# Optimization experiments

Measured on AMD Instinct MI355X. Metric: run time of the kernel, lower is better.

The kernel has to match this reference:

```python
import jax, jax.numpy as jnp
import numpy as np
from jax.ops import segment_sum

N_NODES = 100000
N_EDGES = 3200000
IN_DIM = 128
HID = 128
INT_DIM = 512
OUT_DIM = 3


def gcn_conv(x, W, b, src, dst, n):
    # PyG GCNConv (eval): add self-loops, symmetric normalization, aggregate, bias.
    loop = jnp.arange(n, dtype=src.dtype)
    s = jnp.concatenate([src, loop])
    d = jnp.concatenate([dst, loop])
    deg = segment_sum(jnp.ones_like(d, dtype=x.dtype), d, num_segments=n)  # [N]
    dinv = jnp.where(deg > 0, jax.lax.rsqrt(jnp.maximum(deg, 1e-12)), 0.0)
    norm = dinv[s] * dinv[d]                      # [E+N]
    h = x @ W                                      # [N, F_out]
    msg = h[s] * norm[:, None]                    # gather + scale
    return segment_sum(msg, d, num_segments=n) + b


def setup_inputs() -> dict:
    key = jax.random.key(0)
    ks = jax.random.split(key, 12)
    def lin(kw, kb, fi, fo):
        lim = 1.0 / np.sqrt(fi)
        W = jax.random.uniform(kw, (fi, fo), jnp.float32, -lim, lim)
        b = jax.random.uniform(kb, (fo,), jnp.float32, -lim, lim)
        return W, b
    x = jax.random.normal(ks[0], (N_NODES, IN_DIM), jnp.float32)
    edge_index = jax.random.randint(ks[1], (2, N_EDGES), 0, N_NODES, dtype=jnp.int64)
    W1, b1 = lin(ks[2], ks[3], IN_DIM, HID)
    W2, b2 = lin(ks[4], ks[5], HID, HID)
    W3, b3 = lin(ks[6], ks[7], HID, INT_DIM)
    Wi, bi = lin(ks[8], ks[9], INT_DIM, INT_DIM)
    Wc, bc = lin(ks[10], ks[11], INT_DIM, OUT_DIM)
    return {"x": x, "edge_index": edge_index, "W1": W1, "b1": b1, "W2": W2,
            "b2": b2, "W3": W3, "b3": b3, "Wi": Wi, "bi": bi, "Wc": Wc, "bc": bc}


def reference(x, edge_index, W1, b1, W2, b2, W3, b3, Wi, bi, Wc, bc):
    src, dst = edge_index[0], edge_index[1]
    n = x.shape[0]
    h = jax.nn.relu(gcn_conv(x, W1, b1, src, dst, n))
    h = jax.nn.relu(gcn_conv(h, W2, b2, src, dst, n))
    h = jax.nn.relu(gcn_conv(h, W3, b3, src, dst, n))
    h = jax.nn.relu(h @ Wi + bi)
    return h @ Wc + bc
```

## Files before the change

### kernel.cpp

```cpp
#include <hip/hip_runtime.h>
#include <hip/hip_fp16.h>

#define NN 100000
#define NE 3200000
#define NB 391
#define NBLK 512
#define EPB 6250

typedef unsigned int uint32;
typedef unsigned short u16;
typedef long long ll64;
typedef __attribute__((ext_vector_type(8))) _Float16 half8;
typedef __attribute__((ext_vector_type(4))) float f32x4;

__device__ inline float2 h2f2(uint32 u) {
  __half2 h = *reinterpret_cast<__half2*>(&u);
  return __half22float2(h);
}
__device__ inline uint32 f2h2(float x, float y) {
  return (uint32)__half_as_ushort(__float2half(x)) |
         ((uint32)__half_as_ushort(__float2half(y)) << 16);
}
__device__ inline int edge_at(const void* ei, int is64, ll64 idx) {
  return is64 ? (int)((const ll64*)ei)[idx] : ((const int*)ei)[idx];
}
__device__ inline int detect64(const int* ei32) {
  int acc = 0;
#pragma unroll
  for (int k = 1; k < 32; k += 2) acc |= ei32[k];
  return (acc == 0) ? 1 : 0;
}

__global__ __launch_bounds__(256) void k_binB(const void* __restrict__ ei,
                                              int* __restrict__ tbl) {
  __shared__ int h[NB];
  __shared__ int sIs64;
  int k = blockIdx.x, tid = threadIdx.x;
  for (int i = tid; i < NB; i += 256) h[i] = 0;
  if (tid == 0) sIs64 = detect64((const int*)ei);
  __syncthreads();
  int is64 = sIs64;
  ll64 beg = (ll64)k * EPB, end = beg + EPB;
  for (ll64 i = beg + tid; i < end; i += 256)
    atomicAdd(&h[edge_at(ei, is64, (ll64)NE + i) >> 8], 1);
  __syncthreads();
  for (int i = tid; i < NB; i += 256) tbl[k * NB + i] = h[i];
}
__global__ __launch_bounds__(512) void k_binC1(int* __restrict__ tbl,
                                               int* __restrict__ total) {
  __shared__ int sd[NBLK];
  int b = blockIdx.x, tid = threadIdx.x;
  int v = tbl[tid * NB + b];
  sd[tid] = v;
  __syncthreads();
  for (int off = 1; off < NBLK; off <<= 1) {
    int t = (tid >= off) ? sd[tid - off] : 0;
    __syncthreads();
    sd[tid] += t;
    __syncthreads();
  }
  tbl[tid * NB + b] = sd[tid] - v;
  if (tid == NBLK - 1) total[b] = sd[NBLK - 1];
}
__global__ __launch_bounds__(512) void k_binC2(const int* __restrict__ total,
                                               int* __restrict__ bbase,
                                               int* __restrict__ offs) {
  __shared__ int sd[512];
  int tid = threadIdx.x;
  int v = (tid < NB) ? total[tid] : 0;
  sd[tid] = v;
  __syncthreads();
  for (int off = 1; off < 512; off <<= 1) {
    int t = (tid >= off) ? sd[tid - off] : 0;
    __syncthreads();
    sd[tid] += t;
    __syncthreads();
  }
  if (tid < NB) bbase[tid] = sd[tid] - v;
  if (tid == 0) offs[NN] = NE;
}
__global__ __launch_bounds__(256) void k_binD(const void* __restrict__ ei,
                                              const int* __restrict__ tbl,
                                              const int* __restrict__ bbase,
                                              uint32* __restrict__ binned) {
  __shared__ int lb[NB];
  __shared__ int lc[NB];
  __shared__ int sIs64;
  int k = blockIdx.x, tid = threadIdx.x;
  for (int i = tid; i < NB; i += 256) {
    lb[i] = tbl[k * NB + i] + bbase[i];
    lc[i] = 0;
  }
  if (tid == 0) sIs64 = detect64((const int*)ei);
  __syncthreads();
  int is64 = sIs64;
  ll64 beg = (ll64)k * EPB, end = beg + EPB;
  for (ll64 i = beg + tid; i < end; i += 256) {
    int s = edge_at(ei, is64, i);
    int d = edge_at(ei, is64, (ll64)NE + i);
    int b = d >> 8;
    int r = atomicAdd(&lc[b], 1);
    binned[lb[b] + r] = (uint32)s | ((uint32)(d & 255) << 24);
  }
}
__global__ __launch_bounds__(256) void k_binE(const uint32* __restrict__ binned,
                                              const int* __restrict__ bbase,
                                              const int* __restrict__ total,
                                              int* __restrict__ offs,
                                              float* __restrict__ dinv,
                                              int* __restrict__ csr) {
  __shared__ int cnt[256], pref[256], fil[256];
  int b = blockIdx.x, tid = threadIdx.x;
  cnt[tid] = 0;
  fil[tid] = 0;
  __syncthreads();
  int base = bbase[b], tot = total[b];
  for (int i = tid; i < tot; i += 256) atomicAdd(&cnt[binned[base + i] >> 24], 1);
  __syncthreads();
  int v = cnt[tid];
  pref[tid] = v;
  __syncthreads();
  for (int off = 1; off < 256; off <<= 1) {
    int t = (tid >= off) ? pref[tid - off] : 0;
    __syncthreads();
    pref[tid] += t;
    __syncthreads();
  }
  int myoff = pref[tid] - v;
  pref[tid] = myoff;
  int node = b * 256 + tid;
  if (node < NN) {
    offs[node] = base + myoff;
    dinv[node] = rsqrtf((float)(v + 1));
  }
  __syncthreads();
  for (int i = tid; i < tot; i += 256) {
    uint32 w = binned[base + i];
    int dl = w >> 24;
    int r = atomicAdd(&fil[dl], 1);
    csr[base + pref[dl] + r] = (int)(w & 0xFFFFFFu);
  }
}

__device__ inline void packOne(const float* __restrict__ W, u16* __restrict__ ph,
                               int K, int N, int t) {
  int j = t & 7, lane = (t >> 3) & 63, tl = t >> 9;
  int kbn = K >> 5;
  int kb = tl % kbn, ntile = tl / kbn;
  int k = kb * 32 + (lane >> 4) * 8 + j;
  int n2 = ntile * 16 + (lane & 15);
  ph[t] = __half_as_ushort(__float2half(W[k * N + n2]));
}
__global__ void k_packhalf(const float* W1, const float* W2, const float* W3,
                           const float* Wi, u16* p1, u16* p2, u16* p3, u16* pi,
                           const float4* __restrict__ x, ushort4* __restrict__ xh,
                           const float* __restrict__ dinv) {
  int t = blockIdx.x * blockDim.x + threadIdx.x;
  if (t < 16384) packOne(W1, p1, 128, 128, t);
  else if (t < 32768) packOne(W2, p2, 128, 128, t - 16384);
  else if (t < 98304) packOne(W3, p3, 128, 512, t - 32768);
  else if (t < 360448) packOne(Wi, pi, 512, 512, t - 98304);
  else {
    int i = t - 360448;
    if (i < NN * 32) {
      float4 v = x[i];
      float sc = dinv[i >> 5];
      ushort4 o;
      o.x = __half_as_ushort(__float2half(v.x * sc));
      o.y = __half_as_ushort(__float2half(v.y * sc));
      o.z = __half_as_ushort(__float2half(v.z * sc));
      o.w = __half_as_ushort(__float2half(v.w * sc));
      xh[i] = o;
    }
  }
}

__device__ inline void agg32_phase0(const u16* __restrict__ xin,
                                    const int* __restrict__ csr,
                                    const int* __restrict__ offs,
                                    const float* __restrict__ dinv,
                                    int row0, int tid, u16* __restrict__ tile) {
  int lane = tid & 63, wave = tid >> 6;
  int sub = lane >> 4, fl = lane & 15;
  const uint4* xv = (const uint4*)xin;
#pragma unroll
  for (int rnd = 0; rnd < 2; rnd++) {
    int nloc = rnd * 16 + wave * 4 + sub;
    int node = row0 + nloc;
    int beg = offs[node], end = offs[node + 1];
    float acc[8] = {};
    int j = beg;
    for (; j + 7 < end; j += 8) {
      int s[8];
      uint4 r[8];
#pragma unroll
      for (int q = 0; q < 8; q++) s[q] = csr[j + q];
#pragma unroll
      for (int q = 0; q < 8; q++) r[q] = xv[(ll64)s[q] * 16 + fl];
#pragma unroll
      for (int q = 0; q < 8; q++) {
        float2 p0 = h2f2(r[q].x), p1 = h2f2(r[q].y);
        float2 p2 = h2f2(r[q].z), p3 = h2f2(r[q].w);
        acc[0] += p0.x; acc[1] += p0.y; acc[2] += p1.x; acc[3] += p1.y;
        acc[4] += p2.x; acc[5] += p2.y; acc[6] += p3.x; acc[7] += p3.y;
      }
    }
    for (; j + 3 < end; j += 4) {
      int s[4];
      uint4 r[4];
#pragma unroll
      for (int q = 0; q < 4; q++) s[q] = csr[j + q];
#pragma unroll
      for (int q = 0; q < 4; q++) r[q] = xv[(ll64)s[q] * 16 + fl];
#pragma unroll
      for (int q = 0; q < 4; q++) {
        float2 p0 = h2f2(r[q].x), p1 = h2f2(r[q].y);
        float2 p2 = h2f2(r[q].z), p3 = h2f2(r[q].w);
        acc[0] += p0.x; acc[1] += p0.y; acc[2] += p1.x; acc[3] += p1.y;
        acc[4] += p2.x; acc[5] += p2.y; acc[6] += p3.x; acc[7] += p3.y;
      }
    }
    for (; j < end; j++) {
      uint4 r = xv[(ll64)csr[j] * 16 + fl];
      float2 p0 = h2f2(r.x), p1 = h2f2(r.y), p2 = h2f2(r.z), p3 = h2f2(r.w);
      acc[0] += p0.x; acc[1] += p0.y; acc[2] += p1.x; acc[3] += p1.y;
      acc[4] += p2.x; acc[5] += p2.y; acc[6] += p3.x; acc[7] += p3.y;
    }
    float di = dinv[node];
    uint4 sf = xv[(ll64)node * 16 + fl];
    float2 q0 = h2f2(sf.x), q1 = h2f2(sf.y), q2 = h2f2(sf.z), q3 = h2f2(sf.w);
    uint4 ov;
    ov.x = f2h2(di * (acc[0] + q0.x), di * (acc[1] + q0.y));
    ov.y = f2h2(di * (acc[2] + q1.x), di * (acc[3] + q1.y));
    ov.z = f2h2(di * (acc[4] + q2.x), di * (acc[5] + q2.y));
    ov.w = f2h2(di * (acc[6] + q3.x), di * (acc[7] + q3.y));
    *(uint4*)&tile[nloc * 128 + ((fl ^ (nloc & 7)) << 3)] = ov;
  }
}

__device__ inline void load_af(const u16* __restrict__ tile, int lane,
                               half8 af[2][4]) {
  int quad = (lane >> 4), l16 = lane & 15;
#pragma unroll
  for (int rt = 0; rt < 2; rt++) {
    int row = rt * 16 + l16;
#pragma unroll
    for (int kb = 0; kb < 4; kb++)
      af[rt][kb] = *(const half8*)&tile[row * 128 + (((kb * 4 + quad) ^ (row & 7)) << 3)];
  }
}

__global__ __launch_bounds__(256, 4) void k_fusedL(
    const u16* __restrict__ xin, const int* __restrict__ csr,
    const int* __restrict__ offs, const float* __restrict__ dinv,
    const u16* __restrict__ Wp, const float* __restrict__ bias,
    u16* __restrict__ Co) {
  __shared__ u16 tile[32 * 128];
  int tid = threadIdx.x;
  int wave = tid >> 6, lane = tid & 63, quad = lane >> 4, l16 = lane & 15;
  int row0 = blockIdx.x * 32;
  agg32_phase0(xin, csr, offs, dinv, row0, tid, tile);
  __syncthreads();
  half8 af[2][4];
  load_af(tile, lane, af);
#pragma unroll
  for (int p = 0; p < 2; p++) {
    int nt = wave * 2 + p;
    half8 bv[4];
#pragma unroll
    for (int kb = 0; kb < 4; kb++)
      bv[kb] = *(const half8*)&Wp[((ll64)(nt * 4 + kb) * 64 + lane) * 8];
    f32x4 acc0 = {0, 0, 0, 0}, acc1 = {0, 0, 0, 0};
#pragma unroll
    for (int kb = 0; kb < 4; kb++) {
      acc0 = __builtin_amdgcn_mfma_f32_16x16x32_f16(af[0][kb], bv[kb], acc0, 0, 0, 0);
      acc1 = __builtin_amdgcn_mfma_f32_16x16x32_f16(af[1][kb], bv[kb], acc1, 0, 0, 0);
    }
    int col = nt * 16 + l16;
    float bvv = bias[col];
#pragma unroll
    for (int r = 0; r < 4; r++) {
      int r0 = quad * 4 + r, r1 = r0 + 16;
      Co[(ll64)(row0 + r0) * 128 + col] =
          __half_as_ushort(__float2half(fmaxf(acc0[r] + bvv, 0.0f) * dinv[row0 + r0]));
      Co[(ll64)(row0 + r1) * 128 + col] =
          __half_as_ushort(__float2half(fmaxf(acc1[r] + bvv, 0.0f) * dinv[row0 + r1]));
    }
  }
}

__global__ __launch_bounds__(256, 4) void k_tail32f(
    const u16* __restrict__ xin, const int* __restrict__ csr,
    const int* __restrict__ offs, const float* __restrict__ dinv,
    const u16* __restrict__ W3p, const float* __restrict__ b3,
    const u16* __restrict__ Wip, const float* __restrict__ bi,
    const float* __restrict__ Wc, const float* __restrict__ bc,
    float* __restrict__ out, int M) {
  __shared__ u16 h3s[32 * 512];
  __shared__ float sRed[4][32][3];
  int tid = threadIdx.x;
  int wave = tid >> 6, lane = tid & 63, quad = lane >> 4, l16 = lane & 15;
  int row0 = blockIdx.x * 32;

  agg32_phase0(xin, csr, offs, dinv, row0, tid, h3s);
  __syncthreads();
  half8 af[2][4];
  load_af(h3s, lane, af);
  __syncthreads();

  {
    f32x4 acc0 = {0, 0, 0, 0}, acc1 = {0, 0, 0, 0};
    half8 bq[4];
#pragma unroll
    for (int p = 0; p < 3; p++)
      bq[p] = *(const half8*)&W3p[((ll64)(wave * 32 + p) * 64 + lane) * 8];
#pragma unroll 4
    for (int t = 0; t < 32; t++) {
      if (t + 3 < 32)
        bq[(t + 3) & 3] = *(const half8*)&W3p[((ll64)(wave * 32 + t + 3) * 64 + lane) * 8];
      half8 bcur = bq[t & 3];
      int kb = t & 3;
      acc0 = __builtin_amdgcn_mfma_f32_16x16x32_f16(af[0][kb], bcur, acc0, 0, 0, 0);
      acc1 = __builtin_amdgcn_mfma_f32_16x16x32_f16(af[1][kb], bcur, acc1, 0, 0, 0);
      if (kb == 3) {
        int nt = wave * 8 + (t >> 2);
        int col = nt * 16 + l16;
        float bv = b3[col];
#pragma unroll
        for (int r = 0; r < 4; r++) {
          int row0l = quad * 4 + r;
          float v0 = fmaxf(acc0[r] + bv, 0.0f);
          float v1 = fmaxf(acc1[r] + bv, 0.0f);
          int oct0 = (col >> 3) ^ (row0l & 7);
          h3s[row0l * 512 + oct0 * 8 + (col & 7)] = __half_as_ushort(__float2half(v0));
          int row1l = 16 + row0l;
          int oct1 = (col >> 3) ^ (row1l & 7);
          h3s[row1l * 512 + oct1 * 8 + (col & 7)] = __half_as_ushort(__float2half(v1));
        }
        acc0 = (f32x4){0, 0, 0, 0};
        acc1 = (f32x4){0, 0, 0, 0};
      }
    }
  }
  __syncthreads();

  float acc3[2][4][3] = {};
  {
    f32x4 acc0 = {0, 0, 0, 0}, acc1 = {0, 0, 0, 0};
    half8 bq[4];
#pragma unroll
    for (int p = 0; p < 3; p++)
      bq[p] = *(const half8*)&Wip[((ll64)(wave * 128 + p) * 64 + lane) * 8];
    int r0l = l16, r1l = 16 + l16;
    int sw0 = r0l & 7;
#pragma unroll 4
    for (int t = 0; t < 128; t++) {
      if (t + 3 < 128)
        bq[(t + 3) & 3] = *(const half8*)&Wip[((ll64)(wave * 128 + t + 3) * 64 + lane) * 8];
      half8 bcur = bq[t & 3];
      int kb = t & 15;
      int oct = ((kb * 4 + quad) ^ sw0);
      half8 a0 = *(const half8*)&h3s[r0l * 512 + oct * 8];
      half8 a1 = *(const half8*)&h3s[r1l * 512 + oct * 8];
      acc0 = __builtin_amdgcn_mfma_f32_16x16x32_f16(a0, bcur, acc0, 0, 0, 0);
      acc1 = __builtin_amdgcn_mfma_f32_16x16x32_f16(a1, bcur, acc1, 0, 0, 0);
      if (kb == 15) {
        int nt = wave * 8 + (t >> 4);
        int col = nt * 16 + l16;
        float bv = bi[col];
        float w0 = Wc[col * 3 + 0], w1 = Wc[col * 3 + 1], w2 = Wc[col * 3 + 2];
#pragma unroll
        for (int r = 0; r < 4; r++) {
          float v0 = fmaxf(acc0[r] + bv, 0.0f);
          float v1 = fmaxf(acc1[r] + bv, 0.0f);
          acc3[0][r][0] += v0 * w0; acc3[0][r][1] += v0 * w1; acc3[0][r][2] += v0 * w2;
          acc3[1][r][0] += v1 * w0; acc3[1][r][1] += v1 * w1; acc3[1][r][2] += v1 * w2;
        }
        acc0 = (f32x4){0, 0, 0, 0};
        acc1 = (f32x4){0, 0, 0, 0};
      }
    }
  }
#pragma unroll
  for (int rt = 0; rt < 2; rt++)
#pragma unroll
    for (int r = 0; r < 4; r++)
#pragma unroll
      for (int c = 0; c < 3; c++) {
        float v = acc3[rt][r][c];
        v += __shfl_xor(v, 1);
        v += __shfl_xor(v, 2);
        v += __shfl_xor(v, 4);
        v += __shfl_xor(v, 8);
        acc3[rt][r][c] = v;
      }
  if (l16 == 0) {
#pragma unroll
    for (int rt = 0; rt < 2; rt++)
#pragma unroll
      for (int r = 0; r < 4; r++)
#pragma unroll
        for (int c = 0; c < 3; c++)
          sRed[wave][rt * 16 + quad * 4 + r][c] = acc3[rt][r][c];
  }
  __syncthreads();
  if (tid < 96) {
    int row = tid / 3, c = tid % 3;
    out[(ll64)(row0 + row) * 3 + c] = sRed[0][row][c] + sRed[1][row][c] +
                                      sRed[2][row][c] + sRed[3][row][c] + bc[c];
  }
}

extern "C" void kernel_launch(void* const* d_in, const int* in_sizes, int n_in,
                              void* d_out, int out_size, void* d_ws, size_t ws_size,
                              hipStream_t stream) {
  const float* x  = (const float*)d_in[0];
  const void*  ei = d_in[1];
  const float* W1 = (const float*)d_in[2];
  const float* b1 = (const float*)d_in[3];
  const float* W2 = (const float*)d_in[4];
  const float* b2 = (const float*)d_in[5];
  const float* W3 = (const float*)d_in[6];
  const float* b3 = (const float*)d_in[7];
  const float* Wi = (const float*)d_in[8];
  const float* bi = (const float*)d_in[9];
  const float* Wc = (const float*)d_in[10];
  const float* bc = (const float*)d_in[11];
  float* out = (float*)d_out;

  char* ws = (char*)d_ws;
  const ll64 KB = 1ll << 10, MB = 1ll << 20;
  float* dinv  = (float*)(ws + 0);
  int*   offs  = (int*)(ws + 512 * KB);
  int*   total = (int*)(ws + 1 * MB + 64 * KB);
  int*   bbase = (int*)(ws + 1 * MB + 128 * KB);
  int*   tbl   = (int*)(ws + 1 * MB + 192 * KB);
  uint32* binned = (uint32*)(ws + 2 * MB);
  int*   csr   = (int*)(ws + 15 * MB);
  u16* pW1 = (u16*)(ws + 28 * MB);
  u16* pW2 = (u16*)(ws + 28 * MB + 64 * KB);
  u16* pW3 = (u16*)(ws + 28 * MB + 128 * KB);
  u16* pWi = (u16*)(ws + 28 * MB + 512 * KB);
  u16* xh   = (u16*)(ws + 29 * MB);
  u16* bufA = (u16*)(ws + 55 * MB);
  u16* bufB = (u16*)(ws + 81 * MB);

  const int TB = 256;
  k_binB<<<NBLK, TB, 0, stream>>>(ei, tbl);
  k_binC1<<<NB, NBLK, 0, stream>>>(tbl, total);
  k_binC2<<<1, 512, 0, stream>>>(total, bbase, offs);
  k_binD<<<NBLK, TB, 0, stream>>>(ei, tbl, bbase, binned);
  k_binE<<<NB, TB, 0, stream>>>(binned, bbase, total, offs, dinv, csr);
  k_packhalf<<<(360448 + NN * 32 + TB - 1) / TB, TB, 0, stream>>>(
      W1, W2, W3, Wi, pW1, pW2, pW3, pWi, (const float4*)x, (ushort4*)xh, dinv);

  const int NB32 = NN / 32;

  k_fusedL<<<NB32, TB, 0, stream>>>(xh, csr, offs, dinv, pW1, b1, bufB);
  k_fusedL<<<NB32, TB, 0, stream>>>(bufB, csr, offs, dinv, pW2, b2, bufA);
  k_tail32f<<<NB32, TB, 0, stream>>>(bufA, csr, offs, dinv, pW3, b3, pWi, bi,
                                     Wc, bc, out, NN);
}
```

Baseline: 689.4 us.

## Fold weight packing, bin-base scan and x conversion into existing binning kernels

```diff
diff --git a/kernel.cpp b/kernel.cpp
--- a/kernel.cpp
+++ b/kernel.cpp
@@ -31,11 +31,34 @@
   return (acc == 0) ? 1 : 0;
 }
 
+__device__ inline void packOne(const float* __restrict__ W, u16* __restrict__ ph,
+                               int K, int N, int t) {
+  int j = t & 7, lane = (t >> 3) & 63, tl = t >> 9;
+  int kbn = K >> 5;
+  int kb = tl % kbn, ntile = tl / kbn;
+  int k = kb * 32 + (lane >> 4) * 8 + j;
+  int n2 = ntile * 16 + (lane & 15);
+  ph[t] = __half_as_ushort(__float2half(W[k * N + n2]));
+}
+
 __global__ __launch_bounds__(256) void k_binB(const void* __restrict__ ei,
-                                              int* __restrict__ tbl) {
+                                              int* __restrict__ tbl,
+                                              const float* __restrict__ W1,
+                                              const float* __restrict__ W2,
+                                              const float* __restrict__ W3,
+                                              const float* __restrict__ Wi,
+                                              u16* p1, u16* p2, u16* p3, u16* pi) {
+  int k = blockIdx.x, tid = threadIdx.x;
+  if (k >= NBLK) {
+    int t = (k - NBLK) * 256 + tid;
+    if (t < 16384) packOne(W1, p1, 128, 128, t);
+    else if (t < 32768) packOne(W2, p2, 128, 128, t - 16384);
+    else if (t < 98304) packOne(W3, p3, 128, 512, t - 32768);
+    else packOne(Wi, pi, 512, 512, t - 98304);
+    return;
+  }
   __shared__ int h[NB];
   __shared__ int sIs64;
-  int k = blockIdx.x, tid = threadIdx.x;
   for (int i = tid; i < NB; i += 256) h[i] = 0;
   if (tid == 0) sIs64 = detect64((const int*)ei);
   __syncthreads();
@@ -62,36 +85,32 @@
   tbl[tid * NB + b] = sd[tid] - v;
   if (tid == NBLK - 1) total[b] = sd[NBLK - 1];
 }
-__global__ __launch_bounds__(512) void k_binC2(const int* __restrict__ total,
-                                               int* __restrict__ bbase,
-                                               int* __restrict__ offs) {
-  __shared__ int sd[512];
-  int tid = threadIdx.x;
-  int v = (tid < NB) ? total[tid] : 0;
-  sd[tid] = v;
-  __syncthreads();
-  for (int off = 1; off < 512; off <<= 1) {
-    int t = (tid >= off) ? sd[tid - off] : 0;
-    __syncthreads();
-    sd[tid] += t;
-    __syncthreads();
-  }
-  if (tid < NB) bbase[tid] = sd[tid] - v;
-  if (tid == 0) offs[NN] = NE;
-}
 __global__ __launch_bounds__(256) void k_binD(const void* __restrict__ ei,
                                               const int* __restrict__ tbl,
-                                              const int* __restrict__ bbase,
+                                              const int* __restrict__ total,
                                               uint32* __restrict__ binned) {
   __shared__ int lb[NB];
   __shared__ int lc[NB];
+  __shared__ int s0[NB], s1[NB], sorig[NB];
   __shared__ int sIs64;
   int k = blockIdx.x, tid = threadIdx.x;
   for (int i = tid; i < NB; i += 256) {
-    lb[i] = tbl[k * NB + i] + bbase[i];
+    int v = total[i];
+    sorig[i] = v;
+    s0[i] = v;
     lc[i] = 0;
   }
   if (tid == 0) sIs64 = detect64((const int*)ei);
+  __syncthreads();
+  for (int off = 1; off < NB; off <<= 1) {
+    for (int i = tid; i < NB; i += 256)
+      s1[i] = s0[i] + ((i >= off) ? s0[i - off] : 0);
+    __syncthreads();
+    for (int i = tid; i < NB; i += 256) s0[i] = s1[i];
+    __syncthreads();
+  }
+  for (int i = tid; i < NB; i += 256)
+    lb[i] = tbl[k * NB + i] + s0[i] - sorig[i];
   __syncthreads();
   int is64 = sIs64;
   ll64 beg = (ll64)k * EPB, end = beg + EPB;
@@ -104,17 +123,34 @@
   }
 }
 __global__ __launch_bounds__(256) void k_binE(const uint32* __restrict__ binned,
-                                              const int* __restrict__ bbase,
                                               const int* __restrict__ total,
                                               int* __restrict__ offs,
                                               float* __restrict__ dinv,
-                                              int* __restrict__ csr) {
+                                              int* __restrict__ csr,
+                                              const float4* __restrict__ x,
+                                              ushort4* __restrict__ xh) {
   __shared__ int cnt[256], pref[256], fil[256];
+  __shared__ int s0[NB], s1[NB], sorig[NB];
+  __shared__ float sDinv[256];
   int b = blockIdx.x, tid = threadIdx.x;
+  for (int i = tid; i < NB; i += 256) {
+    int v = total[i];
+    sorig[i] = v;
+    s0[i] = v;
+  }
   cnt[tid] = 0;
   fil[tid] = 0;
   __syncthreads();
-  int base = bbase[b], tot = total[b];
+  for (int off = 1; off < NB; off <<= 1) {
+    for (int i = tid; i < NB; i += 256)
+      s1[i] = s0[i] + ((i >= off) ? s0[i - off] : 0);
+    __syncthreads();
+    for (int i = tid; i < NB; i += 256) s0[i] = s1[i];
+    __syncthreads();
+  }
+  int base = s0[b] - sorig[b];
+  int tot = sorig[b];
+  __syncthreads();
   for (int i = tid; i < tot; i += 256) atomicAdd(&cnt[binned[base + i] >> 24], 1);
   __syncthreads();
   int v = cnt[tid];
@@ -129,10 +165,13 @@
   int myoff = pref[tid] - v;
   pref[tid] = myoff;
   int node = b * 256 + tid;
+  float dv = rsqrtf((float)(v + 1));
+  sDinv[tid] = dv;
   if (node < NN) {
     offs[node] = base + myoff;
-    dinv[node] = rsqrtf((float)(v + 1));
-  }
+    dinv[node] = dv;
+  }
+  if (b == 0 && tid == 0) offs[NN] = NE;
   __syncthreads();
   for (int i = tid; i < tot; i += 256) {
     uint32 w = binned[base + i];
@@ -140,37 +179,18 @@
     int r = atomicAdd(&fil[dl], 1);
     csr[base + pref[dl] + r] = (int)(w & 0xFFFFFFu);
   }
-}
-
-__device__ inline void packOne(const float* __restrict__ W, u16* __restrict__ ph,
-                               int K, int N, int t) {
-  int j = t & 7, lane = (t >> 3) & 63, tl = t >> 9;
-  int kbn = K >> 5;
-  int kb = tl % kbn, ntile = tl / kbn;
-  int k = kb * 32 + (lane >> 4) * 8 + j;
-  int n2 = ntile * 16 + (lane & 15);
-  ph[t] = __half_as_ushort(__float2half(W[k * N + n2]));
-}
-__global__ void k_packhalf(const float* W1, const float* W2, const float* W3,
-                           const float* Wi, u16* p1, u16* p2, u16* p3, u16* pi,
-                           const float4* __restrict__ x, ushort4* __restrict__ xh,
-                           const float* __restrict__ dinv) {
-  int t = blockIdx.x * blockDim.x + threadIdx.x;
-  if (t < 16384) packOne(W1, p1, 128, 128, t);
-  else if (t < 32768) packOne(W2, p2, 128, 128, t - 16384);
-  else if (t < 98304) packOne(W3, p3, 128, 512, t - 32768);
-  else if (t < 360448) packOne(Wi, pi, 512, 512, t - 98304);
-  else {
-    int i = t - 360448;
-    if (i < NN * 32) {
-      float4 v = x[i];
-      float sc = dinv[i >> 5];
+  ll64 slab = (ll64)b * 8192;
+  for (int i = tid; i < 8192; i += 256) {
+    ll64 gi = slab + i;
+    if (gi < (ll64)NN * 32) {
+      float4 vv = x[gi];
+      float sc = sDinv[i >> 5];
       ushort4 o;
-      o.x = __half_as_ushort(__float2half(v.x * sc));
-      o.y = __half_as_ushort(__float2half(v.y * sc));
-      o.z = __half_as_ushort(__float2half(v.z * sc));
-      o.w = __half_as_ushort(__float2half(v.w * sc));
-      xh[i] = o;
+      o.x = __half_as_ushort(__float2half(vv.x * sc));
+      o.y = __half_as_ushort(__float2half(vv.y * sc));
+      o.z = __half_as_ushort(__float2half(vv.z * sc));
+      o.w = __half_as_ushort(__float2half(vv.w * sc));
+      xh[gi] = o;
     }
   }
 }
@@ -433,7 +453,6 @@
   float* dinv  = (float*)(ws + 0);
   int*   offs  = (int*)(ws + 512 * KB);
   int*   total = (int*)(ws + 1 * MB + 64 * KB);
-  int*   bbase = (int*)(ws + 1 * MB + 128 * KB);
   int*   tbl   = (int*)(ws + 1 * MB + 192 * KB);
   uint32* binned = (uint32*)(ws + 2 * MB);
   int*   csr   = (int*)(ws + 15 * MB);
@@ -446,16 +465,13 @@
   u16* bufB = (u16*)(ws + 81 * MB);
 
   const int TB = 256;
-  k_binB<<<NBLK, TB, 0, stream>>>(ei, tbl);
+  k_binB<<<NBLK + 1408, TB, 0, stream>>>(ei, tbl, W1, W2, W3, Wi, pW1, pW2, pW3, pWi);
   k_binC1<<<NB, NBLK, 0, stream>>>(tbl, total);
-  k_binC2<<<1, 512, 0, stream>>>(total, bbase, offs);
-  k_binD<<<NBLK, TB, 0, stream>>>(ei, tbl, bbase, binned);
-  k_binE<<<NB, TB, 0, stream>>>(binned, bbase, total, offs, dinv, csr);
-  k_packhalf<<<(360448 + NN * 32 + TB - 1) / TB, TB, 0, stream>>>(
-      W1, W2, W3, Wi, pW1, pW2, pW3, pWi, (const float4*)x, (ushort4*)xh, dinv);
+  k_binD<<<NBLK, TB, 0, stream>>>(ei, tbl, total, binned);
+  k_binE<<<NB, TB, 0, stream>>>(binned, total, offs, dinv, csr, (const float4*)x,
+                                (ushort4*)xh);
 
   const int NB32 = NN / 32;
-
   k_fusedL<<<NB32, TB, 0, stream>>>(xh, csr, offs, dinv, pW1, b1, bufB);
   k_fusedL<<<NB32, TB, 0, stream>>>(bufB, csr, offs, dinv, pW2, b2, bufA);
   k_tail32f<<<NB32, TB, 0, stream>>>(bufA, csr, offs, dinv, pW3, b3, pWi, bi,
```

New measurement: 704.5 us. 2.2% more time.
